# Performance work log

Measured on AMD Instinct MI355X. Metric: run time of the kernel, lower is better.

The kernel has to match this reference:

```python
import jax, jax.numpy as jnp
import numpy as np

N_NODES = 50000
N_EDGES = 800000
IN_C, HID_C, OUT_C = 256, 512, 256
DROP_P = 0.5


def _glorot(key, fan_in, fan_out):
    lim = float(np.sqrt(6.0 / (fan_in + fan_out)))
    return jax.random.uniform(key, (fan_in, fan_out), jnp.float32, -lim, lim)


def setup_inputs() -> dict:
    key = jax.random.key(0)
    k_x, k_e, k_w1, k_w2 = jax.random.split(key, 4)
    tensor = jax.random.normal(k_x, (N_NODES, IN_C), dtype=jnp.float32)
    edge_index = jax.random.randint(k_e, (2, N_EDGES), 0, N_NODES, dtype=jnp.int64)
    W1 = _glorot(k_w1, IN_C, HID_C)
    b1 = jnp.zeros((HID_C,), jnp.float32)
    W2 = _glorot(k_w2, HID_C, OUT_C)
    b2 = jnp.zeros((OUT_C,), jnp.float32)
    return {"tensor": tensor, "edge_index": edge_index,
            "W1": W1, "b1": b1, "W2": W2, "b2": b2}


def _gcn_conv(x, W, b, row, col, n_nodes):
    # PyG GCNConv: x' = D^-1/2 (A + I) D^-1/2 (x W) + b
    x = x @ W                                            # [N, F_out]
    # degree over targets including self-loops
    deg = jax.ops.segment_sum(jnp.ones_like(col, dtype=x.dtype), col,
                              num_segments=n_nodes) + 1.0
    dinv = jnp.where(deg > 0, jax.lax.rsqrt(deg), 0.0)   # [N]
    norm = dinv[row] * dinv[col]                         # [E]
    msg = x[row] * norm[:, None]                         # [E, F_out] gather
    out = jax.ops.segment_sum(msg, col, num_segments=n_nodes)  # scatter-add
    out = out + x * (dinv * dinv)[:, None]               # self-loop term
    return out + b


def _dropout(x, key, p=DROP_P):
    keep = jax.random.bernoulli(key, 1.0 - p, x.shape)
    return jnp.where(keep, x / (1.0 - p), 0.0)


def reference(tensor, edge_index, W1, b1, W2, b2):
    row, col = edge_index[0], edge_index[1]
    k1, k2 = jax.random.split(jax.random.key(42))
    x = _gcn_conv(tensor, W1, b1, row, col, N_NODES)
    x = _dropout(jax.nn.relu(x), k1)
    x = _gcn_conv(x, W2, b2, row, col, N_NODES)
    x = _dropout(jax.nn.relu(x), k2)
    return x
```

## Files before the change

kernel.cpp:

```cpp
#include <hip/hip_runtime.h>
#include <stdint.h>


#define N_NODES 50000
#define N_EDGES 800000
#define M_PAD   50048
#define IN_C 256
#define HID_C 512
#define OUT_C 256

typedef __attribute__((ext_vector_type(8))) short bf16x8;
typedef __attribute__((ext_vector_type(4))) float f32x4;

struct U2 { unsigned a, b; };

__host__ __device__ constexpr unsigned rotl32(unsigned x, int d) {
  return (x << d) | (x >> (32 - d));
}

#define TF_ROUND(r) { x0 += x1; x1 = rotl32(x1, (r)); x1 ^= x0; }

__host__ __device__ constexpr U2 threefry2x32(unsigned k0, unsigned k1,
                                              unsigned x0, unsigned x1) {
  unsigned ks2 = k0 ^ k1 ^ 0x1BD11BDAu;
  x0 += k0; x1 += k1;
  TF_ROUND(13) TF_ROUND(15) TF_ROUND(26) TF_ROUND(6)  x0 += k1;  x1 += ks2 + 1u;
  TF_ROUND(17) TF_ROUND(29) TF_ROUND(16) TF_ROUND(24) x0 += ks2; x1 += k0 + 2u;
  TF_ROUND(13) TF_ROUND(15) TF_ROUND(26) TF_ROUND(6)  x0 += k0;  x1 += k1 + 3u;
  TF_ROUND(17) TF_ROUND(29) TF_ROUND(16) TF_ROUND(24) x0 += k1;  x1 += ks2 + 4u;
  TF_ROUND(13) TF_ROUND(15) TF_ROUND(26) TF_ROUND(6)  x0 += ks2; x1 += k0 + 5u;
  return U2{x0, x1};
}

__device__ __forceinline__ float drop_apply(float v, unsigned idx, unsigned k0, unsigned k1) {
  v = fmaxf(v, 0.f);
  U2 r = threefry2x32(k0, k1, 0u, idx);
  unsigned bits = r.a ^ r.b;
  return (bits >> 31) ? 0.f : v * 2.0f;
}

__device__ __forceinline__ ushort f2b(float f) {
  unsigned u = __builtin_bit_cast(unsigned, f);
  unsigned r = (u + 0x7fffu + ((u >> 16) & 1u)) >> 16;
  return (ushort)r;
}
__device__ __forceinline__ float b2f(ushort h) {
  unsigned u = (unsigned)h << 16;
  return __builtin_bit_cast(float, u);
}

__device__ __forceinline__ void gload16(const void* g, void* l) {
  __builtin_amdgcn_global_load_lds(
      (const __attribute__((address_space(1))) void*)g,
      (__attribute__((address_space(3))) void*)l, 16, 0, 0);
}

__global__ void deg_kernel(const int* __restrict__ col, int* __restrict__ cnt, int E) {
  int e = blockIdx.x * 256 + threadIdx.x;
  if (e < E) atomicAdd(&cnt[col[e]], 1);
}

__global__ void dinv_kernel(const int* __restrict__ cnt, float* __restrict__ dinv, int N) {
  int n = blockIdx.x * 256 + threadIdx.x;
  if (n < N) dinv[n] = rsqrtf((float)cnt[n] + 1.0f);
}

__global__ __launch_bounds__(1024) void scan_local(const int* __restrict__ cnt,
                                                   int* __restrict__ indptr,
                                                   int* __restrict__ chunkSums, int n) {
  __shared__ int s[1024];
  int gid = blockIdx.x * 1024 + threadIdx.x;
  int v = (gid < n) ? cnt[gid] : 0;
  s[threadIdx.x] = v;
  __syncthreads();
#pragma unroll
  for (int off = 1; off < 1024; off <<= 1) {
    int t = (threadIdx.x >= off) ? s[threadIdx.x - off] : 0;
    __syncthreads();
    s[threadIdx.x] += t;
    __syncthreads();
  }
  if (gid < n) indptr[gid] = s[threadIdx.x] - v;
  if (threadIdx.x == 1023) chunkSums[blockIdx.x] = s[1023];
}

__global__ void scan_chunks(int* __restrict__ chunkSums, int nChunks) {
  if (threadIdx.x == 0 && blockIdx.x == 0) {
    int acc = 0;
    for (int i = 0; i < nChunks; ++i) { int t = chunkSums[i]; chunkSums[i] = acc; acc += t; }
  }
}

__global__ void add_offsets(int* __restrict__ indptr, const int* __restrict__ chunkSums,
                            int n, int total) {
  int gid = blockIdx.x * 256 + threadIdx.x;
  if (gid < n) indptr[gid] += chunkSums[gid >> 10];
  if (gid == 0) indptr[n] = total;
}

__global__ void build_csr(const int* __restrict__ row, const int* __restrict__ col,
                          const int* __restrict__ indptr, int* __restrict__ cursor,
                          int* __restrict__ srcSorted, int E) {
  int e = blockIdx.x * 256 + threadIdx.x;
  if (e < E) {
    int c = col[e];
    int p = indptr[c] + atomicAdd(&cursor[c], 1);
    srcSorted[p] = row[e];
  }
}

__global__ void cvt_f32_bf16(const float* __restrict__ in, ushort* __restrict__ out, int n4) {
  int i = blockIdx.x * 256 + threadIdx.x;
  if (i < n4) {
    float4 v = *(const float4*)(in + (size_t)i * 4);
    ushort4 o = make_ushort4(f2b(v.x), f2b(v.y), f2b(v.z), f2b(v.w));
    *(ushort4*)(out + (size_t)i * 4) = o;
  }
}

template <int LOGK>
__global__ void wT_kernel(const float* __restrict__ W, ushort* __restrict__ WT, int N, int total) {
  int i = blockIdx.x * 256 + threadIdx.x;
  if (i < total) {
    int k = i & ((1 << LOGK) - 1);
    int n = i >> LOGK;
    WT[i] = f2b(W[(size_t)k * N + n]);
  }
}

template <bool EPI>
__global__ __launch_bounds__(256) void gather_agg16(const ushort* __restrict__ X,
                                                    const int* __restrict__ indptr,
                                                    const int* __restrict__ srcS,
                                                    const float* __restrict__ dinv,
                                                    const float* __restrict__ bias,
                                                    void* __restrict__ outp,
                                                    unsigned kk0, unsigned kk1, int N) {
  int wid = (blockIdx.x * 256 + threadIdx.x) >> 6;
  int lane = threadIdx.x & 63;
  if (wid >= N) return;
  int beg = indptr[wid], end = indptr[wid + 1];
  float dc = dinv[wid];
  const int f0 = lane * 4;
  ushort4 sv = *(const ushort4*)(X + (size_t)wid * 256 + f0);
  float a0 = b2f(sv.x) * dc, a1 = b2f(sv.y) * dc,
        a2 = b2f(sv.z) * dc, a3 = b2f(sv.w) * dc;
  int e = beg;
  for (; e + 2 <= end; e += 2) {
    int r0 = srcS[e], r1 = srcS[e + 1];
    float w0 = dinv[r0], w1 = dinv[r1];
    ushort4 v0 = *(const ushort4*)(X + (size_t)r0 * 256 + f0);
    ushort4 v1 = *(const ushort4*)(X + (size_t)r1 * 256 + f0);
    a0 += b2f(v0.x) * w0; a1 += b2f(v0.y) * w0; a2 += b2f(v0.z) * w0; a3 += b2f(v0.w) * w0;
    a0 += b2f(v1.x) * w1; a1 += b2f(v1.y) * w1; a2 += b2f(v1.z) * w1; a3 += b2f(v1.w) * w1;
  }
  if (e < end) {
    int r0 = srcS[e];
    float w0 = dinv[r0];
    ushort4 v0 = *(const ushort4*)(X + (size_t)r0 * 256 + f0);
    a0 += b2f(v0.x) * w0; a1 += b2f(v0.y) * w0; a2 += b2f(v0.z) * w0; a3 += b2f(v0.w) * w0;
  }
  a0 *= dc; a1 *= dc; a2 *= dc; a3 *= dc;
  if (EPI) {
    unsigned base = (unsigned)wid * 256u + (unsigned)f0;
    a0 = drop_apply(a0 + bias[f0 + 0], base + 0, kk0, kk1);
    a1 = drop_apply(a1 + bias[f0 + 1], base + 1, kk0, kk1);
    a2 = drop_apply(a2 + bias[f0 + 2], base + 2, kk0, kk1);
    a3 = drop_apply(a3 + bias[f0 + 3], base + 3, kk0, kk1);
    *(float4*)((float*)outp + (size_t)wid * 256 + f0) = make_float4(a0, a1, a2, a3);
  } else {
    ushort4 o = make_ushort4(f2b(a0), f2b(a1), f2b(a2), f2b(a3));
    *(ushort4*)((ushort*)outp + (size_t)wid * 256 + f0) = o;
  }
}

template <bool EPI, bool BF16OUT>
__global__ __launch_bounds__(256) void gemm_bf16(const ushort* __restrict__ A,
                                                 const ushort* __restrict__ BT,
                                                 void* __restrict__ C,
                                                 int M, int K, int N,
                                                 const float* __restrict__ bias,
                                                 unsigned kk0, unsigned kk1) {
  __shared__ __align__(16) ushort Asm[128 * 32];
  __shared__ __align__(16) ushort Bsm[128 * 32];
  const int tid = threadIdx.x;
  const int lane = tid & 63;
  const int wv = tid >> 6;
  const int wr = wv >> 1, wc = wv & 1;
  const int bm = blockIdx.x * 128;
  const int bn = blockIdx.y * 128;

  f32x4 acc[4][4] = {};

  const ushort* Afb = Asm + (wr * 64 + (lane & 15)) * 32 + (lane >> 4) * 8;
  const ushort* Bfb = Bsm + (wc * 64 + (lane & 15)) * 32 + (lane >> 4) * 8;

  for (int k0 = 0; k0 < K; k0 += 32) {
#pragma unroll
    for (int r = 0; r < 2; ++r) {
      int ei = r * 256 + tid;
      int trow = ei >> 2;
      int tcol = (ei & 3) * 8;
      gload16(A + (size_t)(bm + trow) * K + (k0 + tcol), (void*)(Asm + ei * 8));
      gload16(BT + (size_t)(bn + trow) * K + (k0 + tcol), (void*)(Bsm + ei * 8));
    }
    __syncthreads();
    bf16x8 af[4], bf[4];
#pragma unroll
    for (int i = 0; i < 4; ++i) af[i] = *(const bf16x8*)(Afb + i * 16 * 32);
#pragma unroll
    for (int i = 0; i < 4; ++i) bf[i] = *(const bf16x8*)(Bfb + i * 16 * 32);
#pragma unroll
    for (int m = 0; m < 4; ++m)
#pragma unroll
      for (int n = 0; n < 4; ++n)
        acc[m][n] = __builtin_amdgcn_mfma_f32_16x16x32_bf16(af[m], bf[n], acc[m][n], 0, 0, 0);
    __syncthreads();
  }

  const int rowbase = bm + wr * 64 + ((lane >> 4) << 2);
  const int colbase = bn + wc * 64 + (lane & 15);
#pragma unroll
  for (int m = 0; m < 4; ++m) {
#pragma unroll
    for (int r = 0; r < 4; ++r) {
      int grow = rowbase + m * 16 + r;
#pragma unroll
      for (int n = 0; n < 4; ++n) {
        int gcol = colbase + n * 16;
        float v = acc[m][n][r];
        if (EPI) v = drop_apply(v + bias[gcol], (unsigned)grow * (unsigned)N + (unsigned)gcol, kk0, kk1);
        if (BF16OUT) ((ushort*)C)[(size_t)grow * N + gcol] = f2b(v);
        else         ((float*)C)[(size_t)grow * N + gcol] = v;
      }
    }
  }
}

extern "C" void kernel_launch(void* const* d_in, const int* in_sizes, int n_in,
                              void* d_out, int out_size, void* d_ws, size_t ws_size,
                              hipStream_t stream) {
  const float* x  = (const float*)d_in[0];
  const int*   ei = (const int*)d_in[1];
  const float* W1 = (const float*)d_in[2];
  const float* b1 = (const float*)d_in[3];
  const float* W2 = (const float*)d_in[4];
  const float* b2 = (const float*)d_in[5];
  float* out = (float*)d_out;
  (void)in_sizes; (void)n_in; (void)out_size; (void)ws_size;

  const int* row = ei;
  const int* col = ei + N_EDGES;

  char* ws = (char*)d_ws;
  float*  dinv      = (float*) (ws);
  int*    cnt       = (int*)   (ws + (1u << 18));
  int*    indptr    = (int*)   (ws + (2u << 18));
  int*    cursor    = (int*)   (ws + (3u << 18));
  int*    chunkSums = (int*)   (ws + (4u << 18));
  int*    srcSorted = (int*)   (ws + (4u << 18) + (1u << 16));
  ushort* W1T       = (ushort*)(ws + 5u  * (1u << 20));
  ushort* W2T       = (ushort*)(ws + 6u  * (1u << 20));
  ushort* x16       = (ushort*)(ws + 8u  * (1u << 20));
  ushort* aggB      = (ushort*)(ws + 36u * (1u << 20));
  ushort* h         = (ushort*)(ws + 64u * (1u << 20));
  ushort* hw2       = (ushort*)(ws + 116u* (1u << 20));

  constexpr U2 K1 = threefry2x32(0u, 42u, 0u, 0u);
  constexpr U2 K2 = threefry2x32(0u, 42u, 0u, 1u);

  hipMemsetAsync(cnt, 0, N_NODES * sizeof(int), stream);
  hipMemsetAsync(cursor, 0, N_NODES * sizeof(int), stream);
  deg_kernel<<<(N_EDGES + 255) / 256, 256, 0, stream>>>(col, cnt, N_EDGES);
  dinv_kernel<<<(N_NODES + 255) / 256, 256, 0, stream>>>(cnt, dinv, N_NODES);
  const int nChunks = (N_NODES + 1023) / 1024;
  scan_local<<<nChunks, 1024, 0, stream>>>(cnt, indptr, chunkSums, N_NODES);
  scan_chunks<<<1, 64, 0, stream>>>(chunkSums, nChunks);
  add_offsets<<<(N_NODES + 255) / 256, 256, 0, stream>>>(indptr, chunkSums, N_NODES, N_EDGES);
  build_csr<<<(N_EDGES + 255) / 256, 256, 0, stream>>>(row, col, indptr, cursor, srcSorted, N_EDGES);

  cvt_f32_bf16<<<(N_NODES * IN_C / 4 + 255) / 256, 256, 0, stream>>>(x, x16, N_NODES * IN_C / 4);
  wT_kernel<8><<<(IN_C * HID_C + 255) / 256, 256, 0, stream>>>(W1, W1T, HID_C, IN_C * HID_C);
  wT_kernel<9><<<(HID_C * OUT_C + 255) / 256, 256, 0, stream>>>(W2, W2T, OUT_C, HID_C * OUT_C);
  hipMemsetAsync(aggB + (size_t)N_NODES * IN_C, 0, (size_t)(M_PAD - N_NODES) * IN_C * 2, stream);

  gather_agg16<false><<<(N_NODES + 3) / 4, 256, 0, stream>>>(
      x16, indptr, srcSorted, dinv, nullptr, aggB, 0u, 0u, N_NODES);
  gemm_bf16<true, true><<<dim3(M_PAD / 128, HID_C / 128), 256, 0, stream>>>(
      aggB, W1T, h, M_PAD, IN_C, HID_C, b1, K1.a, K1.b);

  gemm_bf16<false, true><<<dim3(M_PAD / 128, OUT_C / 128), 256, 0, stream>>>(
      h, W2T, hw2, M_PAD, HID_C, OUT_C, nullptr, 0u, 0u);
  gather_agg16<true><<<(N_NODES + 3) / 4, 256, 0, stream>>>(
      hw2, indptr, srcSorted, dinv, b2, out, K2.a, K2.b, N_NODES);
}
```

Baseline: 369.9 us.

## Double-buffer GEMM with swizzled LDS, LDS-staged stores, precomputed dropout mask

```diff
diff --git a/kernel.cpp b/kernel.cpp
--- a/kernel.cpp
+++ b/kernel.cpp
@@ -135,11 +135,13 @@
                                                     const float* __restrict__ dinv,
                                                     const float* __restrict__ bias,
                                                     void* __restrict__ outp,
+                                                    unsigned char* __restrict__ maskOut,
                                                     unsigned kk0, unsigned kk1, int N) {
   int wid = (blockIdx.x * 256 + threadIdx.x) >> 6;
   int lane = threadIdx.x & 63;
   if (wid >= N) return;
-  int beg = indptr[wid], end = indptr[wid + 1];
+  int beg = __builtin_amdgcn_readfirstlane(indptr[wid]);
+  int end = __builtin_amdgcn_readfirstlane(indptr[wid + 1]);
   float dc = dinv[wid];
   const int f0 = lane * 4;
   ushort4 sv = *(const ushort4*)(X + (size_t)wid * 256 + f0);
@@ -171,18 +173,26 @@
   } else {
     ushort4 o = make_ushort4(f2b(a0), f2b(a1), f2b(a2), f2b(a3));
     *(ushort4*)((ushort*)outp + (size_t)wid * 256 + f0) = o;
-  }
-}
-
-template <bool EPI, bool BF16OUT>
+    unsigned gl = (unsigned)wid * 64u + (unsigned)lane;
+    unsigned eb = gl * 8u;
+    unsigned byte = 0;
+#pragma unroll
+    for (int j = 0; j < 8; ++j) {
+      U2 r = threefry2x32(kk0, kk1, 0u, eb + (unsigned)j);
+      byte |= (((r.a ^ r.b) >> 31) & 1u) << j;
+    }
+    maskOut[gl] = (unsigned char)byte;
+  }
+}
+
+template <bool EPI>
 __global__ __launch_bounds__(256) void gemm_bf16(const ushort* __restrict__ A,
                                                  const ushort* __restrict__ BT,
-                                                 void* __restrict__ C,
+                                                 ushort* __restrict__ C,
                                                  int M, int K, int N,
                                                  const float* __restrict__ bias,
-                                                 unsigned kk0, unsigned kk1) {
-  __shared__ __align__(16) ushort Asm[128 * 32];
-  __shared__ __align__(16) ushort Bsm[128 * 32];
+                                                 const unsigned char* __restrict__ mask) {
+  __shared__ __align__(16) ushort lds[4 * 128 * 64];
   const int tid = threadIdx.x;
   const int lane = tid & 63;
   const int wv = tid >> 6;
@@ -191,49 +201,85 @@
   const int bn = blockIdx.y * 128;
 
   f32x4 acc[4][4] = {};
-
-  const ushort* Afb = Asm + (wr * 64 + (lane & 15)) * 32 + (lane >> 4) * 8;
-  const ushort* Bfb = Bsm + (wc * 64 + (lane & 15)) * 32 + (lane >> 4) * 8;
-
-  for (int k0 = 0; k0 < K; k0 += 32) {
-#pragma unroll
-    for (int r = 0; r < 2; ++r) {
-      int ei = r * 256 + tid;
-      int trow = ei >> 2;
-      int tcol = (ei & 3) * 8;
-      gload16(A + (size_t)(bm + trow) * K + (k0 + tcol), (void*)(Asm + ei * 8));
-      gload16(BT + (size_t)(bn + trow) * K + (k0 + tcol), (void*)(Bsm + ei * 8));
+  const int xorv = (lane & 7) << 4;
+
+  auto stage = [&](int buf, int k0) {
+#pragma unroll
+    for (int l = 0; l < 4; ++l) {
+      int cid = l * 256 + tid;
+      int row = cid >> 3;
+      int kcol = ((cid & 7) ^ (row & 7)) * 8;
+      gload16(A + (size_t)(bm + row) * K + k0 + kcol, (void*)(lds + buf * 8192 + cid * 8));
+      gload16(BT + (size_t)(bn + row) * K + k0 + kcol, (void*)(lds + (2 + buf) * 8192 + cid * 8));
+    }
+  };
+
+  const int nt = K >> 6;
+  stage(0, 0);
+  __syncthreads();
+  int cur = 0;
+  for (int t = 0; t < nt; ++t) {
+    if (t + 1 < nt) stage(cur ^ 1, (t + 1) << 6);
+    const char* Ab = (const char*)(lds + cur * 8192);
+    const char* Bb = (const char*)(lds + (2 + cur) * 8192);
+#pragma unroll
+    for (int ks = 0; ks < 2; ++ks) {
+      bf16x8 af[4], bf[4];
+      const int kb = (ks * 64 + (lane >> 4) * 16) ^ xorv;
+#pragma unroll
+      for (int i = 0; i < 4; ++i) {
+        int arow = wr * 64 + i * 16 + (lane & 15);
+        af[i] = *(const bf16x8*)(Ab + arow * 128 + kb);
+        int brow = wc * 64 + i * 16 + (lane & 15);
+        bf[i] = *(const bf16x8*)(Bb + brow * 128 + kb);
+      }
+#pragma unroll
+      for (int m = 0; m < 4; ++m)
+#pragma unroll
+        for (int n = 0; n < 4; ++n)
+          acc[m][n] = __builtin_amdgcn_mfma_f32_16x16x32_bf16(af[m], bf[n], acc[m][n], 0, 0, 0);
     }
     __syncthreads();
-    bf16x8 af[4], bf[4];
-#pragma unroll
-    for (int i = 0; i < 4; ++i) af[i] = *(const bf16x8*)(Afb + i * 16 * 32);
-#pragma unroll
-    for (int i = 0; i < 4; ++i) bf[i] = *(const bf16x8*)(Bfb + i * 16 * 32);
-#pragma unroll
-    for (int m = 0; m < 4; ++m)
-#pragma unroll
-      for (int n = 0; n < 4; ++n)
-        acc[m][n] = __builtin_amdgcn_mfma_f32_16x16x32_bf16(af[m], bf[n], acc[m][n], 0, 0, 0);
-    __syncthreads();
-  }
-
-  const int rowbase = bm + wr * 64 + ((lane >> 4) << 2);
-  const int colbase = bn + wc * 64 + (lane & 15);
+    cur ^= 1;
+  }
+
+  ushort* Csm = (ushort*)lds;
+  const int rowoff = wr * 64 + ((lane >> 4) << 2);
+  const int coloff = wc * 64 + (lane & 15);
+  float bias_v[4];
+  if (EPI) {
+#pragma unroll
+    for (int n = 0; n < 4; ++n) bias_v[n] = bias[bn + coloff + n * 16];
+  }
 #pragma unroll
   for (int m = 0; m < 4; ++m) {
 #pragma unroll
     for (int r = 0; r < 4; ++r) {
-      int grow = rowbase + m * 16 + r;
+      int lrow = rowoff + m * 16 + r;
+      unsigned long long mk = 0;
+      if (EPI) {
+        unsigned base = (unsigned)(bm + lrow) * (unsigned)N + (unsigned)(bn + wc * 64);
+        mk = *(const unsigned long long*)(mask + (base >> 3));
+      }
 #pragma unroll
       for (int n = 0; n < 4; ++n) {
-        int gcol = colbase + n * 16;
         float v = acc[m][n][r];
-        if (EPI) v = drop_apply(v + bias[gcol], (unsigned)grow * (unsigned)N + (unsigned)gcol, kk0, kk1);
-        if (BF16OUT) ((ushort*)C)[(size_t)grow * N + gcol] = f2b(v);
-        else         ((float*)C)[(size_t)grow * N + gcol] = v;
+        if (EPI) {
+          v = fmaxf(v + bias_v[n], 0.f);
+          v = ((mk >> ((lane & 15) + n * 16)) & 1ull) ? 0.f : v * 2.0f;
+        }
+        Csm[lrow * 132 + coloff + n * 16] = f2b(v);
       }
     }
+  }
+  __syncthreads();
+  {
+    int row = tid >> 1, ch = (tid & 1) * 64;
+    const ushort* src = Csm + row * 132 + ch;
+    ushort* dst = C + (size_t)(bm + row) * N + bn + ch;
+#pragma unroll
+    for (int j = 0; j < 8; ++j)
+      *(bf16x8*)(dst + j * 8) = *(const bf16x8*)(src + j * 8);
   }
 }
 
@@ -257,11 +303,12 @@
   int*    cnt       = (int*)   (ws + (1u << 18));
   int*    indptr    = (int*)   (ws + (2u << 18));
   int*    cursor    = (int*)   (ws + (3u << 18));
-  int*    chunkSums = (int*)   (ws + (4u << 18));
-  int*    srcSorted = (int*)   (ws + (4u << 18) + (1u << 16));
+  int*    chunkSums = (int*)   (ws + (1u << 20));
+  int*    srcSorted = (int*)   (ws + (1u << 20) + (1u << 16));
   ushort* W1T       = (ushort*)(ws + 5u  * (1u << 20));
-  ushort* W2T       = (ushort*)(ws + 6u  * (1u << 20));
-  ushort* x16       = (ushort*)(ws + 8u  * (1u << 20));
+  ushort* W2T       = (ushort*)(ws + 5u  * (1u << 20) + (1u << 19));
+  unsigned char* mask1 = (unsigned char*)(ws + 6u * (1u << 20));
+  ushort* x16       = (ushort*)(ws + 10u * (1u << 20));
   ushort* aggB      = (ushort*)(ws + 36u * (1u << 20));
   ushort* h         = (ushort*)(ws + 64u * (1u << 20));
   ushort* hw2       = (ushort*)(ws + 116u* (1u << 20));
@@ -285,12 +332,12 @@
   hipMemsetAsync(aggB + (size_t)N_NODES * IN_C, 0, (size_t)(M_PAD - N_NODES) * IN_C * 2, stream);
 
   gather_agg16<false><<<(N_NODES + 3) / 4, 256, 0, stream>>>(
-      x16, indptr, srcSorted, dinv, nullptr, aggB, 0u, 0u, N_NODES);
-  gemm_bf16<true, true><<<dim3(M_PAD / 128, HID_C / 128), 256, 0, stream>>>(
-      aggB, W1T, h, M_PAD, IN_C, HID_C, b1, K1.a, K1.b);
-
-  gemm_bf16<false, true><<<dim3(M_PAD / 128, OUT_C / 128), 256, 0, stream>>>(
-      h, W2T, hw2, M_PAD, HID_C, OUT_C, nullptr, 0u, 0u);
+      x16, indptr, srcSorted, dinv, nullptr, aggB, mask1, K1.a, K1.b, N_NODES);
+  gemm_bf16<true><<<dim3(M_PAD / 128, HID_C / 128), 256, 0, stream>>>(
+      aggB, W1T, h, M_PAD, IN_C, HID_C, b1, mask1);
+
+  gemm_bf16<false><<<dim3(M_PAD / 128, OUT_C / 128), 256, 0, stream>>>(
+      h, W2T, hw2, M_PAD, HID_C, OUT_C, nullptr, nullptr);
   gather_agg16<true><<<(N_NODES + 3) / 4, 256, 0, stream>>>(
-      hw2, indptr, srcSorted, dinv, b2, out, K2.a, K2.b, N_NODES);
-}
+      hw2, indptr, srcSorted, dinv, b2, out, nullptr, K2.a, K2.b, N_NODES);
+}
```

After: 347.4 us. 1.06x faster.
